# Kernel optimization log

Measured on AMD Instinct MI355X. Metric: run time of the kernel, lower is better.

The kernel has to match this reference:

```python
import jax, jax.numpy as jnp
import numpy as np


def normalize_adj(adj):
    """Symmetrize (adj + adj.T*(adj.T>adj) - adj*(adj.T>adj)), add self loops, row-normalize D^-1 A."""
    at = jnp.swapaxes(adj, -1, -2)
    mask = (at > adj).astype(adj.dtype)
    a = adj + at * mask - adj * mask
    m = a.shape[-1]
    a = a + jnp.eye(m, dtype=a.dtype)
    rowsum = a.sum(axis=-1, keepdims=True)
    inv = jnp.where(rowsum > 0, 1.0 / rowsum, 0.0)
    return a * inv


def setup_inputs() -> dict:
    key = jax.random.key(0)
    ks = jax.random.split(key, 8)
    N, n, T, dim, M = 4, 3, 512, 2048, 256
    x = jax.random.normal(ks[0], (N, n, T, dim), dtype=jnp.float32)
    nodes = jax.random.normal(ks[1], (N, M, dim), dtype=jnp.float32)
    adj = (jax.random.uniform(ks[2], (N, M, M)) < 0.05).astype(jnp.float32)
    conv_w = jax.random.normal(ks[3], (2048, dim, 3), dtype=jnp.float32) * 0.02  # OIH
    conv_b = jnp.zeros((2048,), dtype=jnp.float32)
    W1 = jax.random.normal(ks[4], (dim, dim), dtype=jnp.float32) * 0.02
    b1 = jnp.zeros((dim,), dtype=jnp.float32)
    W2 = jax.random.normal(ks[5], (dim, dim), dtype=jnp.float32) * 0.02
    b2 = jnp.zeros((dim,), dtype=jnp.float32)
    return {"x": x, "nodes": nodes, "adj": adj, "conv_w": conv_w, "conv_b": conv_b,
            "W1": W1, "b1": b1, "W2": W2, "b2": b2}


def reference(x, nodes, adj, conv_w, conv_b, W1, b1, W2, b2):
    N, n, T, dim = x.shape
    # Conv1d front-end: (N*n, C=dim, T), kernel 3, pad 1, then ReLU
    feats = x.reshape(N * n, T, dim).transpose(0, 2, 1)  # [B, C, T]
    feats = jax.lax.conv_general_dilated(
        feats, conv_w, window_strides=(1,), padding=[(1, 1)],
        dimension_numbers=("NCH", "OIH", "NCH"))
    feats = jax.nn.relu(feats + conv_b[None, :, None])
    feats = feats.transpose(0, 2, 1).reshape(N, n, T, dim)
    # GCN_Module over per-sample node graphs (batched over N)
    a = normalize_adj(adj)                                   # [N, M, M]
    h = jax.nn.relu(jnp.einsum("bij,bjf->bif", a, nodes @ W1) + b1)
    out = jnp.einsum("bij,bjf->bif", a, h @ W2) + b2         # [N, M, dim]
    return feats, out
```

## Files before the change

### kernel.cpp

```cpp
#include <hip/hip_runtime.h>
#include <stdint.h>

typedef __bf16 bf16x8 __attribute__((ext_vector_type(8)));
typedef float floatx4 __attribute__((ext_vector_type(4)));

__device__ __forceinline__ void gload_lds16(const void* g, void* l) {
    __builtin_amdgcn_global_load_lds((const __attribute__((address_space(1))) void*)g,
                                     (__attribute__((address_space(3))) void*)l, 16, 0, 0);
}

__device__ __forceinline__ uint16_t f2bf(float f) {
    uint32_t u = __float_as_uint(f);
    u += 0x7fff + ((u >> 16) & 1);
    return (uint16_t)(u >> 16);
}
__device__ __forceinline__ uint32_t f2bf2(float lo, float hi) {
    return (uint32_t)f2bf(lo) | ((uint32_t)f2bf(hi) << 16);
}

#define PREP_NP 24672
#define PREP_NW 26720
#define PREP_NT 28768
#define PREP_NF 32864
#define PREP_NA 33888

__global__ __launch_bounds__(256)
void k_prep(const float* __restrict__ x, uint32_t* __restrict__ xpad,
            const float* __restrict__ w, uint16_t* __restrict__ wT,
            const float* __restrict__ W1, const float* __restrict__ W2,
            uint16_t* __restrict__ W1T, uint16_t* __restrict__ W2T,
            const float* __restrict__ nodes, uint32_t* __restrict__ nodesb,
            const float* __restrict__ adj, float* __restrict__ aval,
            uint16_t* __restrict__ aidx, int* __restrict__ annz)
{
    __shared__ union {
        float wbuf[6144];
        float tile[64][65];
        struct { float part[4]; int wcnt[4]; int woff[4]; float sinv; } na;
    } sm;
    const int bid = blockIdx.x;
    const int tid = threadIdx.x;

    if (bid < PREP_NP) {
        int idx2 = bid * 256 + tid;
        int i2   = idx2 & 1023;
        int tmp  = idx2 >> 10;
        int b    = tmp / 514;
        int tt   = tmp - b * 514;
        float lo = 0.0f, hi = 0.0f;
        if (tt >= 1 && tt <= 512) {
            const float* s = x + ((size_t)(b * 512 + tt - 1) << 11) + i2 * 2;
            lo = s[0]; hi = s[1];
        }
        xpad[idx2] = f2bf2(lo, hi);
    } else if (bid < PREP_NW) {
        int o = bid - PREP_NP;
        const float* src = w + (size_t)o * 6144;
        uint16_t*    dst = wT + (size_t)o * 6144;
        #pragma unroll
        for (int it = 0; it < 24; ++it)
            sm.wbuf[it * 256 + tid] = src[it * 256 + tid];
        __syncthreads();
        #pragma unroll
        for (int h = 0; h < 3; ++h)
            #pragma unroll
            for (int c = 0; c < 8; ++c) {
                int i = c * 256 + tid;
                dst[h * 2048 + i] = f2bf(sm.wbuf[i * 3 + h]);
            }
    } else if (bid < PREP_NT) {
        int t  = bid - PREP_NW;
        int z  = t >> 10;
        int by = (t >> 5) & 31;
        int bx = t & 31;
        const float* src = z ? W2 : W1;
        uint16_t*    dst = z ? W2T : W1T;
        int tx = tid & 63, ty = tid >> 6;
        for (int rr = ty; rr < 64; rr += 4)
            sm.tile[rr][tx] = src[(size_t)(by * 64 + rr) * 2048 + bx * 64 + tx];
        __syncthreads();
        for (int rr = ty; rr < 64; rr += 4)
            dst[(size_t)(bx * 64 + rr) * 2048 + by * 64 + tx] = f2bf(sm.tile[tx][rr]);
    } else if (bid < PREP_NF) {
        int idx2 = (bid - PREP_NT) * 256 + tid;
        nodesb[idx2] = f2bf2(nodes[idx2 * 2], nodes[idx2 * 2 + 1]);
    } else {
        int t = bid - PREP_NF;
        int i = t & 255, b = t >> 8, j = tid;
        const float* A = adj + ((size_t)b << 16);
        float aij = A[(i << 8) + j];
        float aji = A[(j << 8) + i];
        float v = fmaxf(aij, aji);
        if (j == i) v += 1.0f;

        float s = v;
        #pragma unroll
        for (int off = 32; off > 0; off >>= 1) s += __shfl_down(s, off);

        bool pred = v != 0.0f;
        unsigned long long m = __ballot(pred);
        int wid = j >> 6;
        if ((j & 63) == 0) { sm.na.part[wid] = s; sm.na.wcnt[wid] = (int)__popcll(m); }
        __syncthreads();
        int row = (b << 8) + i;
        if (j == 0) {
            float tt = sm.na.part[0] + sm.na.part[1] + sm.na.part[2] + sm.na.part[3];
            sm.na.sinv = tt > 0.0f ? 1.0f / tt : 0.0f;
            int o = 0;
            #pragma unroll
            for (int ww = 0; ww < 4; ++ww) { sm.na.woff[ww] = o; o += sm.na.wcnt[ww]; }
            annz[row] = o;
        }
        __syncthreads();
        if (pred) {
            int pos = sm.na.woff[wid] + (int)__popcll(m & ((1ull << (j & 63)) - 1ull));
            aval[row * 256 + pos] = v * sm.na.sinv;
            aidx[row * 256 + pos] = (uint16_t)j;
        }
    }
}

template<bool CONV, int SPLIT>
__global__ __launch_bounds__(256)
void k_gemm(const uint16_t* __restrict__ A, const uint16_t* __restrict__ BT,
            float* __restrict__ C, const float* __restrict__ bias,
            int M, int N, int K, int relu)
{
    __shared__ __align__(16) uint16_t As[128 * 32];
    __shared__ __align__(16) uint16_t Bs[128 * 32];
    const int tid  = threadIdx.x;
    const int rt   = blockIdx.y * 128;
    const int ct   = blockIdx.x * 128;
    const int lane = tid & 63;
    const int wave = tid >> 6;
    const int wm   = (wave >> 1) * 64;
    const int wn   = (wave & 1) * 64;
    const int lm   = lane & 15;
    const int kq   = (lane >> 4) * 8;
    const int srow  = tid >> 2;
    const int skcol = (tid & 3) * 8;

    const int kchunk = K / SPLIT;
    const int kbeg   = (SPLIT > 1) ? blockIdx.z * kchunk : 0;
    const size_t MN  = (size_t)M * N;

    floatx4 acc[4][4] = {};

    for (int k0 = kbeg; k0 < kbeg + kchunk; k0 += 32) {
        #pragma unroll
        for (int ii = 0; ii < 2; ++ii) {
            int row = ii * 64 + srow;
            const uint16_t* gsrc;
            if (CONV) {
                int r  = rt + row;
                int b  = r >> 9;
                int t  = r & 511;
                int kk = k0 + skcol;
                int h  = kk >> 11;
                int ic = kk & 2047;
                gsrc = A + ((size_t)(b * 514 + t + h) << 11) + ic;
            } else {
                gsrc = A + (size_t)(rt + row) * K + k0 + skcol;
            }
            gload_lds16(gsrc, &As[ii * 2048 + tid * 8]);
            gload_lds16(BT + (size_t)(ct + row) * K + k0 + skcol, &Bs[ii * 2048 + tid * 8]);
        }
        __syncthreads();

        bf16x8 af[4], bfr[4];
        #pragma unroll
        for (int mt = 0; mt < 4; ++mt)
            af[mt] = *(const bf16x8*)&As[(wm + mt * 16 + lm) * 32 + kq];
        #pragma unroll
        for (int nt = 0; nt < 4; ++nt)
            bfr[nt] = *(const bf16x8*)&Bs[(wn + nt * 16 + lm) * 32 + kq];
        #pragma unroll
        for (int mt = 0; mt < 4; ++mt)
            #pragma unroll
            for (int nt = 0; nt < 4; ++nt)
                acc[mt][nt] = __builtin_amdgcn_mfma_f32_16x16x32_bf16(af[mt], bfr[nt], acc[mt][nt], 0, 0, 0);
        __syncthreads();
    }

    const int lq = lane >> 4;
    #pragma unroll
    for (int mt = 0; mt < 4; ++mt) {
        #pragma unroll
        for (int nt = 0; nt < 4; ++nt) {
            int col = ct + wn + nt * 16 + lm;
            float bv = (SPLIT == 1 && bias) ? bias[col] : 0.0f;
            #pragma unroll
            for (int r = 0; r < 4; ++r) {
                int row = rt + wm + mt * 16 + lq * 4 + r;
                if (SPLIT == 1) {
                    float v = acc[mt][nt][r] + bv;
                    if (relu) v = fmaxf(v, 0.0f);
                    C[(size_t)row * N + col] = v;
                } else {
                    C[blockIdx.z * MN + (size_t)row * N + col] = acc[mt][nt][r];
                }
            }
        }
    }
}

__global__ void k_reduce4(const float4* __restrict__ hp, float4* __restrict__ h) {
    int i = blockIdx.x * 256 + threadIdx.x;
    float4 a = hp[i], b = hp[i + 524288], c = hp[i + 1048576], d = hp[i + 1572864];
    float4 r;
    r.x = a.x + b.x + c.x + d.x;
    r.y = a.y + b.y + c.y + d.y;
    r.z = a.z + b.z + c.z + d.z;
    r.w = a.w + b.w + c.w + d.w;
    h[i] = r;
}

template<bool RELU, bool OUTBF>
__global__ void k_amul(const float* __restrict__ aval, const uint16_t* __restrict__ aidx,
                       const int* __restrict__ annz, const float* __restrict__ H,
                       const float* __restrict__ bias, void* __restrict__ outp)
{
    int f = blockIdx.x * 256 + threadIdx.x;
    int i = blockIdx.y;
    int b = blockIdx.z;
    int row = (b << 8) + i;
    __shared__ float vv[256];
    __shared__ int   jj[256];
    int n0 = annz[row];
    vv[threadIdx.x] = aval[row * 256 + threadIdx.x];
    jj[threadIdx.x] = aidx[row * 256 + threadIdx.x];
    __syncthreads();
    const float* Hb = H + ((size_t)b << 8) * 2048;
    float s = 0.0f;
    #pragma unroll 4
    for (int c = 0; c < n0; ++c)
        s += vv[c] * Hb[(size_t)jj[c] * 2048 + f];
    s += bias[f];
    if (RELU) s = fmaxf(s, 0.0f);
    size_t off = ((size_t)row) * 2048 + f;
    if (OUTBF) ((uint16_t*)outp)[off] = f2bf(s);
    else       ((float*)outp)[off]    = s;
}


extern "C" void kernel_launch(void* const* d_in, const int* in_sizes, int n_in,
                              void* d_out, int out_size, void* d_ws, size_t ws_size,
                              hipStream_t stream)
{
    const float* x      = (const float*)d_in[0];
    const float* nodes  = (const float*)d_in[1];
    const float* adj    = (const float*)d_in[2];
    const float* conv_w = (const float*)d_in[3];
    const float* conv_b = (const float*)d_in[4];
    const float* W1     = (const float*)d_in[5];
    const float* b1     = (const float*)d_in[6];
    const float* W2     = (const float*)d_in[7];
    const float* b2     = (const float*)d_in[8];
    float* out = (float*)d_out;

    char* ws = (char*)d_ws;
    uint16_t* xpad   = (uint16_t*)(ws);
    uint16_t* wmT    = (uint16_t*)(ws + 25288704);
    uint16_t* W1T    = (uint16_t*)(ws + 50454528);
    uint16_t* W2T    = (uint16_t*)(ws + 58843136);
    uint16_t* nodesb = (uint16_t*)(ws + 67231744);
    float*    aval   = (float*)   (ws + 71426048);
    float*    h1     = (float*)   (ws + 72474624);
    uint16_t* hb     = (uint16_t*)(ws + 80863232);
    float*    h2     = (float*)   (ws + 85057536);
    uint16_t* aidx   = (uint16_t*)(ws + 93446144);
    int*      annz   = (int*)     (ws + 93970432);
    float*    hp     = (float*)   (ws);

    k_prep<<<PREP_NA, 256, 0, stream>>>(x, (uint32_t*)xpad, conv_w, wmT,
                                        W1, W2, W1T, W2T,
                                        nodes, (uint32_t*)nodesb,
                                        adj, aval, aidx, annz);

    k_gemm<true, 1><<<dim3(16, 48), 256, 0, stream>>>(xpad, wmT, out, conv_b, 6144, 2048, 6144, 1);
    k_gemm<false, 4><<<dim3(16, 8, 4), 256, 0, stream>>>(nodesb, W1T, hp, nullptr, 1024, 2048, 2048, 0);
    k_reduce4<<<2048, 256, 0, stream>>>((const float4*)hp, (float4*)h1);
    k_amul<true, true><<<dim3(8, 256, 4), 256, 0, stream>>>(aval, aidx, annz, h1, b1, hb);
    k_gemm<false, 4><<<dim3(16, 8, 4), 256, 0, stream>>>(hb, W2T, hp, nullptr, 1024, 2048, 2048, 0);
    k_reduce4<<<2048, 256, 0, stream>>>((const float4*)hp, (float4*)h2);
    k_amul<false, false><<<dim3(8, 256, 4), 256, 0, stream>>>(aval, aidx, annz, h2, b2, out + 12582912);
}
```

Before: 475.2 us.

## Reassociate GCN as (A·X)·W, drop split-K reduce, reorder prep blocks

The GCN layers are reassociated so the sparse normalized adjacency multiplies the input first (A·nodes, then A·h), with bias and ReLU folded into a new 64x64-tile GEMM epilogue. This removes the split-K partial buffers, the two reduction kernels and the nodes bf16 conversion. The prep kernel is reordered so the adjacency-normalization blocks run first, and the conv GEMM precomputes per-row base addresses outside the K loop. The risk is that the 64-tile GEMM has lower per-block reuse and the aggregation now reads raw fp32 inputs, with slightly different rounding order.

```diff
diff --git a/kernel.cpp b/kernel.cpp
--- a/kernel.cpp
+++ b/kernel.cpp
@@ -18,18 +18,16 @@
     return (uint32_t)f2bf(lo) | ((uint32_t)f2bf(hi) << 16);
 }
 
-#define PREP_NP 24672
-#define PREP_NW 26720
-#define PREP_NT 28768
-#define PREP_NF 32864
-#define PREP_NA 33888
+#define PREP_A  1024
+#define PREP_W  3072
+#define PREP_T  5120
+#define PREP_N  29792
 
 __global__ __launch_bounds__(256)
 void k_prep(const float* __restrict__ x, uint32_t* __restrict__ xpad,
             const float* __restrict__ w, uint16_t* __restrict__ wT,
             const float* __restrict__ W1, const float* __restrict__ W2,
             uint16_t* __restrict__ W1T, uint16_t* __restrict__ W2T,
-            const float* __restrict__ nodes, uint32_t* __restrict__ nodesb,
             const float* __restrict__ adj, float* __restrict__ aval,
             uint16_t* __restrict__ aidx, int* __restrict__ annz)
 {
@@ -41,8 +39,68 @@
     const int bid = blockIdx.x;
     const int tid = threadIdx.x;
 
-    if (bid < PREP_NP) {
-        int idx2 = bid * 256 + tid;
+    if (bid < PREP_A) {
+        int i = bid & 255, b = bid >> 8, j = tid;
+        const float* A = adj + ((size_t)b << 16);
+        float aij = A[(i << 8) + j];
+        float aji = A[(j << 8) + i];
+        float v = fmaxf(aij, aji);
+        if (j == i) v += 1.0f;
+
+        float s = v;
+        #pragma unroll
+        for (int off = 32; off > 0; off >>= 1) s += __shfl_down(s, off);
+
+        bool pred = v != 0.0f;
+        unsigned long long m = __ballot(pred);
+        int wid = j >> 6;
+        if ((j & 63) == 0) { sm.na.part[wid] = s; sm.na.wcnt[wid] = (int)__popcll(m); }
+        __syncthreads();
+        int row = (b << 8) + i;
+        if (j == 0) {
+            float tt = sm.na.part[0] + sm.na.part[1] + sm.na.part[2] + sm.na.part[3];
+            sm.na.sinv = tt > 0.0f ? 1.0f / tt : 0.0f;
+            int o = 0;
+            #pragma unroll
+            for (int ww = 0; ww < 4; ++ww) { sm.na.woff[ww] = o; o += sm.na.wcnt[ww]; }
+            annz[row] = o;
+        }
+        __syncthreads();
+        if (pred) {
+            int pos = sm.na.woff[wid] + (int)__popcll(m & ((1ull << (j & 63)) - 1ull));
+            aval[row * 256 + pos] = v * sm.na.sinv;
+            aidx[row * 256 + pos] = (uint16_t)j;
+        }
+    } else if (bid < PREP_W) {
+        int o = bid - PREP_A;
+        const float* src = w + (size_t)o * 6144;
+        uint16_t*    dst = wT + (size_t)o * 6144;
+        #pragma unroll
+        for (int it = 0; it < 24; ++it)
+            sm.wbuf[it * 256 + tid] = src[it * 256 + tid];
+        __syncthreads();
+        #pragma unroll
+        for (int h = 0; h < 3; ++h)
+            #pragma unroll
+            for (int c = 0; c < 8; ++c) {
+                int i = c * 256 + tid;
+                dst[h * 2048 + i] = f2bf(sm.wbuf[i * 3 + h]);
+            }
+    } else if (bid < PREP_T) {
+        int t  = bid - PREP_W;
+        int z  = t >> 10;
+        int by = (t >> 5) & 31;
+        int bx = t & 31;
+        const float* src = z ? W2 : W1;
+        uint16_t*    dst = z ? W2T : W1T;
+        int tx = tid & 63, ty = tid >> 6;
+        for (int rr = ty; rr < 64; rr += 4)
+            sm.tile[rr][tx] = src[(size_t)(by * 64 + rr) * 2048 + bx * 64 + tx];
+        __syncthreads();
+        for (int rr = ty; rr < 64; rr += 4)
+            dst[(size_t)(bx * 64 + rr) * 2048 + by * 64 + tx] = f2bf(sm.tile[tx][rr]);
+    } else {
+        int idx2 = (bid - PREP_T) * 256 + tid;
         int i2   = idx2 & 1023;
         int tmp  = idx2 >> 10;
         int b    = tmp / 514;
@@ -53,78 +111,14 @@
             lo = s[0]; hi = s[1];
         }
         xpad[idx2] = f2bf2(lo, hi);
-    } else if (bid < PREP_NW) {
-        int o = bid - PREP_NP;
-        const float* src = w + (size_t)o * 6144;
-        uint16_t*    dst = wT + (size_t)o * 6144;
-        #pragma unroll
-        for (int it = 0; it < 24; ++it)
-            sm.wbuf[it * 256 + tid] = src[it * 256 + tid];
-        __syncthreads();
-        #pragma unroll
-        for (int h = 0; h < 3; ++h)
-            #pragma unroll
-            for (int c = 0; c < 8; ++c) {
-                int i = c * 256 + tid;
-                dst[h * 2048 + i] = f2bf(sm.wbuf[i * 3 + h]);
-            }
-    } else if (bid < PREP_NT) {
-        int t  = bid - PREP_NW;
-        int z  = t >> 10;
-        int by = (t >> 5) & 31;
-        int bx = t & 31;
-        const float* src = z ? W2 : W1;
-        uint16_t*    dst = z ? W2T : W1T;
-        int tx = tid & 63, ty = tid >> 6;
-        for (int rr = ty; rr < 64; rr += 4)
-            sm.tile[rr][tx] = src[(size_t)(by * 64 + rr) * 2048 + bx * 64 + tx];
-        __syncthreads();
-        for (int rr = ty; rr < 64; rr += 4)
-            dst[(size_t)(bx * 64 + rr) * 2048 + by * 64 + tx] = f2bf(sm.tile[tx][rr]);
-    } else if (bid < PREP_NF) {
-        int idx2 = (bid - PREP_NT) * 256 + tid;
-        nodesb[idx2] = f2bf2(nodes[idx2 * 2], nodes[idx2 * 2 + 1]);
-    } else {
-        int t = bid - PREP_NF;
-        int i = t & 255, b = t >> 8, j = tid;
-        const float* A = adj + ((size_t)b << 16);
-        float aij = A[(i << 8) + j];
-        float aji = A[(j << 8) + i];
-        float v = fmaxf(aij, aji);
-        if (j == i) v += 1.0f;
-
-        float s = v;
-        #pragma unroll
-        for (int off = 32; off > 0; off >>= 1) s += __shfl_down(s, off);
-
-        bool pred = v != 0.0f;
-        unsigned long long m = __ballot(pred);
-        int wid = j >> 6;
-        if ((j & 63) == 0) { sm.na.part[wid] = s; sm.na.wcnt[wid] = (int)__popcll(m); }
-        __syncthreads();
-        int row = (b << 8) + i;
-        if (j == 0) {
-            float tt = sm.na.part[0] + sm.na.part[1] + sm.na.part[2] + sm.na.part[3];
-            sm.na.sinv = tt > 0.0f ? 1.0f / tt : 0.0f;
-            int o = 0;
-            #pragma unroll
-            for (int ww = 0; ww < 4; ++ww) { sm.na.woff[ww] = o; o += sm.na.wcnt[ww]; }
-            annz[row] = o;
-        }
-        __syncthreads();
-        if (pred) {
-            int pos = sm.na.woff[wid] + (int)__popcll(m & ((1ull << (j & 63)) - 1ull));
-            aval[row * 256 + pos] = v * sm.na.sinv;
-            aidx[row * 256 + pos] = (uint16_t)j;
-        }
-    }
-}
-
-template<bool CONV, int SPLIT>
+    }
+}
+
+template<bool CONV, bool RELU>
 __global__ __launch_bounds__(256)
 void k_gemm(const uint16_t* __restrict__ A, const uint16_t* __restrict__ BT,
             float* __restrict__ C, const float* __restrict__ bias,
-            int M, int N, int K, int relu)
+            int N, int K)
 {
     __shared__ __align__(16) uint16_t As[128 * 32];
     __shared__ __align__(16) uint16_t Bs[128 * 32];
@@ -140,30 +134,28 @@
     const int srow  = tid >> 2;
     const int skcol = (tid & 3) * 8;
 
-    const int kchunk = K / SPLIT;
-    const int kbeg   = (SPLIT > 1) ? blockIdx.z * kchunk : 0;
-    const size_t MN  = (size_t)M * N;
+    size_t abase[2], bbase[2];
+    #pragma unroll
+    for (int ii = 0; ii < 2; ++ii) {
+        int row = ii * 64 + srow;
+        if (CONV) {
+            int r = rt + row;
+            int b = r >> 9;
+            int t = r & 511;
+            abase[ii] = ((size_t)(b * 514 + t) << 11) + skcol;
+        } else {
+            abase[ii] = (size_t)(rt + row) * K + skcol;
+        }
+        bbase[ii] = (size_t)(ct + row) * K + skcol;
+    }
 
     floatx4 acc[4][4] = {};
 
-    for (int k0 = kbeg; k0 < kbeg + kchunk; k0 += 32) {
+    for (int k0 = 0; k0 < K; k0 += 32) {
         #pragma unroll
         for (int ii = 0; ii < 2; ++ii) {
-            int row = ii * 64 + srow;
-            const uint16_t* gsrc;
-            if (CONV) {
-                int r  = rt + row;
-                int b  = r >> 9;
-                int t  = r & 511;
-                int kk = k0 + skcol;
-                int h  = kk >> 11;
-                int ic = kk & 2047;
-                gsrc = A + ((size_t)(b * 514 + t + h) << 11) + ic;
-            } else {
-                gsrc = A + (size_t)(rt + row) * K + k0 + skcol;
-            }
-            gload_lds16(gsrc, &As[ii * 2048 + tid * 8]);
-            gload_lds16(BT + (size_t)(ct + row) * K + k0 + skcol, &Bs[ii * 2048 + tid * 8]);
+            gload_lds16(A  + abase[ii] + k0, &As[ii * 2048 + tid * 8]);
+            gload_lds16(BT + bbase[ii] + k0, &Bs[ii * 2048 + tid * 8]);
         }
         __syncthreads();
 
@@ -188,37 +180,84 @@
         #pragma unroll
         for (int nt = 0; nt < 4; ++nt) {
             int col = ct + wn + nt * 16 + lm;
-            float bv = (SPLIT == 1 && bias) ? bias[col] : 0.0f;
+            float bv = bias[col];
             #pragma unroll
             for (int r = 0; r < 4; ++r) {
                 int row = rt + wm + mt * 16 + lq * 4 + r;
-                if (SPLIT == 1) {
-                    float v = acc[mt][nt][r] + bv;
-                    if (relu) v = fmaxf(v, 0.0f);
-                    C[(size_t)row * N + col] = v;
-                } else {
-                    C[blockIdx.z * MN + (size_t)row * N + col] = acc[mt][nt][r];
-                }
+                float v = acc[mt][nt][r] + bv;
+                if (RELU) v = fmaxf(v, 0.0f);
+                C[(size_t)row * N + col] = v;
             }
         }
     }
 }
 
-__global__ void k_reduce4(const float4* __restrict__ hp, float4* __restrict__ h) {
-    int i = blockIdx.x * 256 + threadIdx.x;
-    float4 a = hp[i], b = hp[i + 524288], c = hp[i + 1048576], d = hp[i + 1572864];
-    float4 r;
-    r.x = a.x + b.x + c.x + d.x;
-    r.y = a.y + b.y + c.y + d.y;
-    r.z = a.z + b.z + c.z + d.z;
-    r.w = a.w + b.w + c.w + d.w;
-    h[i] = r;
-}
-
-template<bool RELU, bool OUTBF>
+template<bool RELU>
+__global__ __launch_bounds__(256)
+void k_gemm64(const uint16_t* __restrict__ A, const uint16_t* __restrict__ BT,
+              float* __restrict__ C, const float* __restrict__ bias,
+              int N, int K)
+{
+    __shared__ __align__(16) uint16_t As[64 * 32];
+    __shared__ __align__(16) uint16_t Bs[64 * 32];
+    const int tid  = threadIdx.x;
+    const int rt   = blockIdx.y * 64;
+    const int ct   = blockIdx.x * 64;
+    const int lane = tid & 63;
+    const int wave = tid >> 6;
+    const int wm   = (wave >> 1) * 32;
+    const int wn   = (wave & 1) * 32;
+    const int lm   = lane & 15;
+    const int kq   = (lane >> 4) * 8;
+    const int srow  = tid >> 2;
+    const int skcol = (tid & 3) * 8;
+
+    const size_t abase = (size_t)(rt + srow) * K + skcol;
+    const size_t bbase = (size_t)(ct + srow) * K + skcol;
+
+    floatx4 acc[2][2] = {};
+
+    for (int k0 = 0; k0 < K; k0 += 32) {
+        gload_lds16(A  + abase + k0, &As[tid * 8]);
+        gload_lds16(BT + bbase + k0, &Bs[tid * 8]);
+        __syncthreads();
+
+        bf16x8 af[2], bfr[2];
+        #pragma unroll
+        for (int mt = 0; mt < 2; ++mt)
+            af[mt] = *(const bf16x8*)&As[(wm + mt * 16 + lm) * 32 + kq];
+        #pragma unroll
+        for (int nt = 0; nt < 2; ++nt)
+            bfr[nt] = *(const bf16x8*)&Bs[(wn + nt * 16 + lm) * 32 + kq];
+        #pragma unroll
+        for (int mt = 0; mt < 2; ++mt)
+            #pragma unroll
+            for (int nt = 0; nt < 2; ++nt)
+                acc[mt][nt] = __builtin_amdgcn_mfma_f32_16x16x32_bf16(af[mt], bfr[nt], acc[mt][nt], 0, 0, 0);
+        __syncthreads();
+    }
+
+    const int lq = lane >> 4;
+    #pragma unroll
+    for (int mt = 0; mt < 2; ++mt) {
+        #pragma unroll
+        for (int nt = 0; nt < 2; ++nt) {
+            int col = ct + wn + nt * 16 + lm;
+            float bv = bias[col];
+            #pragma unroll
+            for (int r = 0; r < 4; ++r) {
+                int row = rt + wm + mt * 16 + lq * 4 + r;
+                float v = acc[mt][nt][r] + bv;
+                if (RELU) v = fmaxf(v, 0.0f);
+                C[(size_t)row * N + col] = v;
+            }
+        }
+    }
+}
+
 __global__ void k_amul(const float* __restrict__ aval, const uint16_t* __restrict__ aidx,
                        const int* __restrict__ annz, const float* __restrict__ H,
-                       const float* __restrict__ bias, void* __restrict__ outp)
+                       uint16_t* __restrict__ outp)
 {
     int f = blockIdx.x * 256 + threadIdx.x;
     int i = blockIdx.y;
@@ -235,11 +274,7 @@
     #pragma unroll 4
     for (int c = 0; c < n0; ++c)
         s += vv[c] * Hb[(size_t)jj[c] * 2048 + f];
-    s += bias[f];
-    if (RELU) s = fmaxf(s, 0.0f);
-    size_t off = ((size_t)row) * 2048 + f;
-    if (OUTBF) ((uint16_t*)outp)[off] = f2bf(s);
-    else       ((float*)outp)[off]    = s;
+    outp[(size_t)row * 2048 + f] = f2bf(s);
 }
 
 
@@ -263,25 +298,21 @@
     uint16_t* wmT    = (uint16_t*)(ws + 25288704);
     uint16_t* W1T    = (uint16_t*)(ws + 50454528);
     uint16_t* W2T    = (uint16_t*)(ws + 58843136);
-    uint16_t* nodesb = (uint16_t*)(ws + 67231744);
-    float*    aval   = (float*)   (ws + 71426048);
-    float*    h1     = (float*)   (ws + 72474624);
-    uint16_t* hb     = (uint16_t*)(ws + 80863232);
-    float*    h2     = (float*)   (ws + 85057536);
-    uint16_t* aidx   = (uint16_t*)(ws + 93446144);
-    int*      annz   = (int*)     (ws + 93970432);
-    float*    hp     = (float*)   (ws);
-
-    k_prep<<<PREP_NA, 256, 0, stream>>>(x, (uint32_t*)xpad, conv_w, wmT,
-                                        W1, W2, W1T, W2T,
-                                        nodes, (uint32_t*)nodesb,
-                                        adj, aval, aidx, annz);
-
-    k_gemm<true, 1><<<dim3(16, 48), 256, 0, stream>>>(xpad, wmT, out, conv_b, 6144, 2048, 6144, 1);
-    k_gemm<false, 4><<<dim3(16, 8, 4), 256, 0, stream>>>(nodesb, W1T, hp, nullptr, 1024, 2048, 2048, 0);
-    k_reduce4<<<2048, 256, 0, stream>>>((const float4*)hp, (float4*)h1);
-    k_amul<true, true><<<dim3(8, 256, 4), 256, 0, stream>>>(aval, aidx, annz, h1, b1, hb);
-    k_gemm<false, 4><<<dim3(16, 8, 4), 256, 0, stream>>>(hb, W2T, hp, nullptr, 1024, 2048, 2048, 0);
-    k_reduce4<<<2048, 256, 0, stream>>>((const float4*)hp, (float4*)h2);
-    k_amul<false, false><<<dim3(8, 256, 4), 256, 0, stream>>>(aval, aidx, annz, h2, b2, out + 12582912);
-}
+    float*    aval   = (float*)   (ws + 67231744);
+    uint16_t* aidx   = (uint16_t*)(ws + 68280320);
+    int*      annz   = (int*)     (ws + 68804608);
+    uint16_t* gbf    = (uint16_t*)(ws + 68808704);
+    float*    h      = (float*)   (ws + 73003008);
+    uint16_t* ahb    = (uint16_t*)(ws + 81391616);
+
+    k_prep<<<PREP_N, 256, 0, stream>>>(x, (uint32_t*)xpad, conv_w, wmT,
+                                       W1, W2, W1T, W2T,
+                                       adj, aval, aidx, annz);
+
+    k_gemm<true, true><<<dim3(16, 48), 256, 0, stream>>>(xpad, wmT, out, conv_b, 2048, 6144);
+
+    k_amul<<<dim3(8, 256, 4), 256, 0, stream>>>(aval, aidx, annz, nodes, gbf);
+    k_gemm64<true><<<dim3(32, 16), 256, 0, stream>>>(gbf, W1T, h, b1, 2048, 2048);
+    k_amul<<<dim3(8, 256, 4), 256, 0, stream>>>(aval, aidx, annz, h, ahb);
+    k_gemm64<false><<<dim3(32, 16), 256, 0, stream>>>(ahb, W2T, out + 12582912, b2, 2048, 2048);
+}
```

New measurement: 470.1 us. Within noise of the previous version (-1.1%).
